# Kernel optimization log

Measured on AMD Instinct MI355X. Metric: run time of the kernel, lower is better.

## Reference

```python
import jax, jax.numpy as jnp
import numpy as np

EMBED_DIM = 512
KERNEL = 17


def setup_inputs() -> dict:
    key = jax.random.key(0)
    ks = jax.random.split(key, 5)
    B, L, C = 2, 8192, EMBED_DIM
    s = C ** -0.5
    x = jax.random.normal(ks[0], (B, L, C), dtype=jnp.float32)
    # weights stored as (in, out); equivalent to torch Linear weight.T
    w_qkv = jax.random.normal(ks[1], (C, 3 * C), dtype=jnp.float32) * s
    w_width = jax.random.normal(ks[2], (C, 1), dtype=jnp.float32) * s
    b_width = jax.random.normal(ks[3], (1,), dtype=jnp.float32) * 0.01
    w_out = jax.random.normal(ks[4], (C, C), dtype=jnp.float32) * s
    return {"x": x, "w_qkv": w_qkv, "w_width": w_width, "b_width": b_width, "w_out": w_out}


def reference(x, w_qkv, w_width, b_width, w_out):
    B, L, C = x.shape
    K = KERNEL
    half_k = K // 2
    scale = C ** -0.5

    qkv = x @ w_qkv                      # [B,L,3C]
    q, k, v = jnp.split(qkv, 3, axis=-1)

    # learned soft window width in [1, K]
    width = jax.nn.sigmoid(x @ w_width + b_width) * (K - 1) + 1.0   # [B,L,1]

    # sliding windows of k/v: pad along L then gather K-sized windows
    k_pad = jnp.pad(k, ((0, 0), (half_k, half_k), (0, 0)))
    v_pad = jnp.pad(v, ((0, 0), (half_k, half_k), (0, 0)))
    idx = jnp.arange(L)[:, None] + jnp.arange(K)[None, :]           # [L,K]
    k_win = k_pad[:, idx]                # [B,L,K,C]
    v_win = v_pad[:, idx]                # [B,L,K,C]

    scores = jnp.einsum('blc,blkc->blk', q, k_win) * scale          # [B,L,K]

    rel_pos = jnp.abs(jnp.arange(K, dtype=jnp.float32) - half_k)    # [K]
    soft_mask = jax.nn.sigmoid((width - rel_pos) * 5.0)             # [B,L,K]
    scores = scores - (1.0 - soft_mask) * 10000.0

    attn = jax.nn.softmax(scores, axis=-1)
    out = jnp.einsum('blk,blkc->blc', attn, v_win)                  # [B,L,C]
    return (out + v) @ w_out
```

## Files before the change

kernel.cpp:

```cpp
#include <hip/hip_runtime.h>

typedef unsigned short u16;
typedef unsigned int   u32;
typedef __attribute__((ext_vector_type(8))) short          shortx8;
typedef __attribute__((ext_vector_type(8))) unsigned short ushortx8;
typedef __attribute__((ext_vector_type(4))) float          floatx4;

#define AS1 __attribute__((address_space(1)))
#define AS3 __attribute__((address_space(3)))

#define SEG 8208
#define LV  16416

__device__ __forceinline__ float b2f(u16 v) {
  return __uint_as_float(((u32)v) << 16);
}
__device__ __forceinline__ u16 f2b(float f) {
  u32 u = __float_as_uint(f);
  u += 0x7FFF + ((u >> 16) & 1);
  return (u16)(u >> 16);
}
__device__ __forceinline__ void cp16(const void* g, void* l) {
  __builtin_amdgcn_global_load_lds((AS1 u32*)g, (AS3 u32*)l, 16, 0, 0);
}

__global__ __launch_bounds__(256)
void prep(const float* __restrict__ x, const float* __restrict__ w_width,
          const float* __restrict__ b_width, const float* __restrict__ w_qkv,
          const float* __restrict__ w_out, u16* __restrict__ xb,
          float* __restrict__ width, u16* __restrict__ wqkvT,
          u16* __restrict__ woutT, u16* __restrict__ Vt) {
  __shared__ u16 tile[32][33];
  const int b = blockIdx.x;
  if (b < 4096) {
    const int lane = threadIdx.x & 63;
    const int row  = b * 4 + (threadIdx.x >> 6);
    const float* xp = x + (size_t)row * 512 + lane * 8;
    floatx4 v0 = *(const floatx4*)xp;
    floatx4 v1 = *(const floatx4*)(xp + 4);
    floatx4 w0 = *(const floatx4*)(w_width + lane * 8);
    floatx4 w1 = *(const floatx4*)(w_width + lane * 8 + 4);
    float s = 0.f;
    ushortx8 o;
#pragma unroll
    for (int j = 0; j < 4; ++j) {
      s += v0[j] * w0[j] + v1[j] * w1[j];
      o[j] = f2b(v0[j]); o[4 + j] = f2b(v1[j]);
    }
    *(ushortx8*)(xb + (size_t)row * 512 + lane * 8) = o;
#pragma unroll
    for (int m = 32; m >= 1; m >>= 1) s += __shfl_xor(s, m, 64);
    if (lane == 0)
      width[row] = 16.f / (1.f + __expf(-(s + b_width[0]))) + 1.f;
  } else if (b < 5120) {
    const float* in; u16* out; int R, C, t;
    if (b < 4864) { in = w_qkv; out = wqkvT; R = 512; C = 1536; t = b - 4096; }
    else          { in = w_out; out = woutT; R = 512; C = 512;  t = b - 4864; }
    const int nbx = C / 32;
    const int cb = (t % nbx) * 32;
    const int rb = (t / nbx) * 32;
    const int tx = threadIdx.x & 31;
    const int ty = threadIdx.x >> 5;
#pragma unroll
    for (int i = 0; i < 32; i += 8)
      tile[ty + i][tx] = f2b(in[(size_t)(rb + ty + i) * C + cb + tx]);
    __syncthreads();
#pragma unroll
    for (int i = 0; i < 32; i += 8)
      out[(size_t)(cb + ty + i) * R + rb + tx] = tile[tx][ty + i];
  } else {
    const int idx = (b - 5120) * 256 + threadIdx.x;
    const int ch = idx >> 5;
    const int k  = idx & 31;
    const int seg = k >> 4;
    const int j   = k & 15;
    const int col = seg * SEG + (j < 8 ? j : 8192 + j);
    Vt[(size_t)ch * LV + col] = 0;
  }
}

template <int MODE>
__global__ __launch_bounds__(256, 3)
void gemm_bt(const u16* __restrict__ A, const u16* __restrict__ Bt,
             void* __restrict__ C0, u16* __restrict__ Kb, u16* __restrict__ Vt) {
  const int K = 512;
  __shared__ alignas(16) u16 lds[17408];
  u16* As = lds;
  u16* Bs = lds + 8192;
  const int tid  = threadIdx.x;
  const int lane = tid & 63;
  const int wave = tid >> 6;
  const int quad = lane >> 4;
  const int lr   = lane & 15;
  const int row0 = blockIdx.x * 128;
  const int col0 = blockIdx.y * 128;
  const int wr   = (wave >> 1) * 64;
  const int wc   = (wave & 1) * 64;

  floatx4 acc[4][4];
#pragma unroll
  for (int i = 0; i < 4; ++i)
#pragma unroll
    for (int j = 0; j < 4; ++j) acc[i][j] = (floatx4)0.0f;

  int srow[4], scol[4];
#pragma unroll
  for (int p = 0; p < 4; ++p) {
    int c = p * 256 + tid;
    srow[p] = c >> 3;
    scol[p] = ((c & 7) ^ (srow[p] & 7)) * 8;
  }
  const int swz = lr & 7;

  for (int k0 = 0; k0 < K; k0 += 64) {
#pragma unroll
    for (int p = 0; p < 4; ++p)
      cp16(A + (size_t)(row0 + srow[p]) * K + k0 + scol[p], &As[(p * 256 + tid) * 8]);
#pragma unroll
    for (int p = 0; p < 4; ++p)
      cp16(Bt + (size_t)(col0 + srow[p]) * K + k0 + scol[p], &Bs[(p * 256 + tid) * 8]);
    __syncthreads();

#pragma unroll
    for (int ks = 0; ks < 2; ++ks) {
      shortx8 af[4], bf[4];
#pragma unroll
      for (int mi = 0; mi < 4; ++mi)
        af[mi] = *(const shortx8*)
            &As[((wr + mi * 16 + lr) * 8 + ((ks * 4 + quad) ^ swz)) * 8];
#pragma unroll
      for (int ni = 0; ni < 4; ++ni)
        bf[ni] = *(const shortx8*)
            &Bs[((wc + ni * 16 + lr) * 8 + ((ks * 4 + quad) ^ swz)) * 8];
#pragma unroll
      for (int mi = 0; mi < 4; ++mi)
#pragma unroll
        for (int ni = 0; ni < 4; ++ni)
          acc[mi][ni] = __builtin_amdgcn_mfma_f32_16x16x32_bf16(
              af[mi], bf[ni], acc[mi][ni], 0, 0, 0);
    }
    __syncthreads();
  }

  if constexpr (MODE == 1) {
    if (col0 < 1024) {
      u16* dst = (col0 < 512) ? (u16*)C0 : Kb;
      const int cb = col0 & 511;
#pragma unroll
      for (int mi = 0; mi < 4; ++mi)
#pragma unroll
        for (int ni = 0; ni < 4; ++ni)
#pragma unroll
          for (int r = 0; r < 4; ++r)
            lds[(wr + mi * 16 + quad * 4 + r) * 136 + wc + ni * 16 + lr] =
                f2b(acc[mi][ni][r]);
      __syncthreads();
      const int rr = tid >> 4, cc = (tid & 15) * 8;
#pragma unroll
      for (int it = 0; it < 8; ++it) {
        int row = it * 16 + rr;
        *(ushortx8*)(dst + (size_t)(row0 + row) * 512 + cb + cc) =
            *(const ushortx8*)&lds[row * 136 + cc];
      }
    } else {
      const int cb = col0 - 1024;
      const int bb = row0 >> 13, pib0 = row0 & 8191;
#pragma unroll
      for (int mi = 0; mi < 4; ++mi)
#pragma unroll
        for (int ni = 0; ni < 4; ++ni)
#pragma unroll
          for (int r = 0; r < 4; ++r)
            lds[(wc + ni * 16 + lr) * 136 + wr + mi * 16 + quad * 4 + r] =
                f2b(acc[mi][ni][r]);
      __syncthreads();
      const int rr = tid >> 4, cc = (tid & 15) * 8;
#pragma unroll
      for (int it = 0; it < 8; ++it) {
        int chl = it * 16 + rr;
        ushortx8 v = *(const ushortx8*)&lds[chl * 136 + cc];
        *(ushortx8*)(Vt + (size_t)(cb + chl) * LV + (size_t)bb * SEG + 8 + pib0 + cc) = v;
      }
    }
  } else {
    float* Cf = (float*)C0;
#pragma unroll
    for (int mi = 0; mi < 4; ++mi)
#pragma unroll
      for (int ni = 0; ni < 4; ++ni)
#pragma unroll
        for (int r = 0; r < 4; ++r) {
          int row = row0 + wr + mi * 16 + quad * 4 + r;
          int col = col0 + wc + ni * 16 + lr;
          Cf[(size_t)row * 512 + col] = acc[mi][ni][r];
        }
  }
}

__global__ __launch_bounds__(256, 2)
void attn_fused(const u16* __restrict__ Q, const u16* __restrict__ Kb,
                const u16* __restrict__ Vt, const float* __restrict__ width,
                const u16* __restrict__ woutT, float* __restrict__ Out) {
  __shared__ alignas(16) u16 Osw[32 * 512];
  __shared__ float S[32][33];
  __shared__ u16 P[32][40];
  const int tid  = threadIdx.x;
  const int lane = tid & 63;
  const int wave = tid >> 6;
  const int quad = lane >> 4;
  const int lr   = lane & 15;
  const int p0   = blockIdx.x * 32;
  const int rg   = wave & 1;
  const int tw   = wave >> 1;
  const int prg  = p0 + rg * 16;
  const int pib  = prg & 8191;
  const int bb   = prg >> 13;

  floatx4 s0 = (floatx4)0.0f;
#pragma unroll 4
  for (int s = 0; s < 16; ++s) {
    const int k0 = s * 32 + quad * 8;
    shortx8 af = *(const shortx8*)(Q  + (size_t)(prg + lr) * 512 + k0);
    shortx8 f  = *(const shortx8*)(Kb +
                   (ptrdiff_t)(prg - 8 + tw * 16 + lr) * 512 + k0);
    s0 = __builtin_amdgcn_mfma_f32_16x16x32_bf16(af, f, s0, 0, 0, 0);
  }
#pragma unroll
  for (int r = 0; r < 4; ++r)
    S[rg * 16 + quad * 4 + r][tw * 16 + lr] = s0[r];
  __syncthreads();

  {
    const int row = tid >> 3, cg = tid & 7;
    const int rr  = row & 15;
    const int pibr = (p0 + (row >> 4) * 16) & 8191;
    const float scale = 0.044194173824159216f;
    const float wrow = width[p0 + row];
    float sv[4]; float mx = -1e30f;
#pragma unroll
    for (int t = 0; t < 4; ++t) {
      const int col = t * 8 + cg;
      const int d  = col - rr;
      const int jb = pibr + col - 8;
      float rel = fabsf((float)(d - 8));
      float msk = 1.f / (1.f + __expf(-5.f * (wrow - rel)));
      float pen = (1.f - msk) * 10000.f;
      float val = (d >= 0 && d <= 16)
          ? (((unsigned)jb < 8192u ? S[row][col] * scale : 0.f) - pen)
          : -1e30f;
      sv[t] = val; mx = fmaxf(mx, val);
    }
#pragma unroll
    for (int m = 4; m >= 1; m >>= 1) mx = fmaxf(mx, __shfl_xor(mx, m, 64));
    float e[4], sum = 0.f;
#pragma unroll
    for (int t = 0; t < 4; ++t) { e[t] = __expf(sv[t] - mx); sum += e[t]; }
#pragma unroll
    for (int m = 4; m >= 1; m >>= 1) sum += __shfl_xor(sum, m, 64);
    const float inv = 1.f / sum;
#pragma unroll
    for (int t = 0; t < 4; ++t) {
      const int col = t * 8 + cg;
      P[row][col] = f2b(e[t] * inv + ((col - rr) == 8 ? 1.f : 0.f));
    }
  }
  __syncthreads();

  shortx8 pf = *(const shortx8*)&P[rg * 16 + lr][quad * 8];
  const size_t cb0 = (size_t)bb * SEG + pib;
#pragma unroll 4
  for (int ctl = 0; ctl < 16; ++ctl) {
    const int ch = tw * 256 + ctl * 16 + lr;
    shortx8 vf = *(const shortx8*)(Vt + (size_t)ch * LV + cb0 + quad * 8);
    floatx4 o = __builtin_amdgcn_mfma_f32_16x16x32_bf16(pf, vf, (floatx4)0.0f,
                                                        0, 0, 0);
    const int c = tw * 32 + ctl * 2 + (lr >> 3);
#pragma unroll
    for (int r = 0; r < 4; ++r) {
      const int row = rg * 16 + quad * 4 + r;
      Osw[row * 512 + (((c & ~7) | ((c & 7) ^ (row & 7))) << 3) + (lr & 7)] =
          f2b(o[r]);
    }
  }
  __syncthreads();

  const int wc = wave * 128;
  floatx4 acc[2][8];
#pragma unroll
  for (int mi = 0; mi < 2; ++mi)
#pragma unroll
    for (int ni = 0; ni < 8; ++ni) acc[mi][ni] = (floatx4)0.0f;

  for (int ksl = 0; ksl < 16; ++ksl) {
    const int kg = ksl * 32 + quad * 8;
    shortx8 bfr[8], afr[2];
#pragma unroll
    for (int ni = 0; ni < 8; ++ni)
      bfr[ni] = *(const shortx8*)(woutT + (size_t)(wc + ni * 16 + lr) * 512 + kg);
#pragma unroll
    for (int mi = 0; mi < 2; ++mi) {
      const int row = mi * 16 + lr;
      const int c = ksl * 4 + quad;
      afr[mi] = *(const shortx8*)
          &Osw[row * 512 + (((c & ~7) | ((c & 7) ^ (row & 7))) << 3)];
    }
#pragma unroll
    for (int mi = 0; mi < 2; ++mi)
#pragma unroll
      for (int ni = 0; ni < 8; ++ni)
        acc[mi][ni] = __builtin_amdgcn_mfma_f32_16x16x32_bf16(
            afr[mi], bfr[ni], acc[mi][ni], 0, 0, 0);
  }

#pragma unroll
  for (int mi = 0; mi < 2; ++mi)
#pragma unroll
    for (int ni = 0; ni < 8; ++ni)
#pragma unroll
      for (int r = 0; r < 4; ++r)
        Out[(size_t)(p0 + mi * 16 + quad * 4 + r) * 512 + wc + ni * 16 + lr] =
            acc[mi][ni][r];
}

extern "C" void kernel_launch(void* const* d_in, const int* in_sizes, int n_in,
                              void* d_out, int out_size, void* d_ws, size_t ws_size,
                              hipStream_t stream) {
  const float* x       = (const float*)d_in[0];
  const float* w_qkv   = (const float*)d_in[1];
  const float* w_width = (const float*)d_in[2];
  const float* b_width = (const float*)d_in[3];
  const float* w_out   = (const float*)d_in[4];
  float* out = (float*)d_out;

  const int M = 16384, N3 = 1536;
  char* ws = (char*)d_ws;
  u16*   xb    = (u16*)(ws);
  u16*   Qb    = (u16*)(ws + 16777216);
  u16*   Kb    = (u16*)(ws + 33554432 + 8192);
  u16*   Vt    = (u16*)(ws + 50348032);
  u16*   wqkvT = (u16*)(ws + 67158016);
  u16*   woutT = (u16*)(ws + 68730880);
  float* width = (float*)(ws + 69255168);

  dim3 blk(256);
  prep<<<dim3(5184), blk, 0, stream>>>(x, w_width, b_width, w_qkv, w_out,
                                       xb, width, wqkvT, woutT, Vt);
  gemm_bt<1><<<dim3(M / 128, N3 / 128), blk, 0, stream>>>(xb, wqkvT, Qb, Kb, Vt);
  attn_fused<<<dim3(M / 32), blk, 0, stream>>>(Qb, Kb, Vt, width, woutT, out);
}
```

Measured before the change: 164.9 us.

## Double attn_fused block to 512 threads with split-K scores and register prefetch

The fused attention kernel now runs 8 waves per block instead of 4. The QK^T score computation is split across two K halves, with partial sums kept in shared memory and added during the softmax. The PV and output-projection work is spread over twice as many waves, each doing half as much. The output GEMM also prefetches the next K-slice of w_out fragments into registers to hide load latency. This aims to raise per-block parallelism and latency hiding, at the cost of extra shared memory for the partial scores and lower register budget per thread under the 512,4 launch bounds.

```diff
diff --git a/kernel.cpp b/kernel.cpp
--- a/kernel.cpp
+++ b/kernel.cpp
@@ -197,12 +197,12 @@
   }
 }
 
-__global__ __launch_bounds__(256, 2)
+__global__ __launch_bounds__(512, 4)
 void attn_fused(const u16* __restrict__ Q, const u16* __restrict__ Kb,
                 const u16* __restrict__ Vt, const float* __restrict__ width,
                 const u16* __restrict__ woutT, float* __restrict__ Out) {
   __shared__ alignas(16) u16 Osw[32 * 512];
-  __shared__ float S[32][33];
+  __shared__ float Sp[2][32][33];
   __shared__ u16 P[32][40];
   const int tid  = threadIdx.x;
   const int lane = tid & 63;
@@ -211,92 +211,104 @@
   const int lr   = lane & 15;
   const int p0   = blockIdx.x * 32;
   const int rg   = wave & 1;
-  const int tw   = wave >> 1;
+  const int tw   = (wave >> 1) & 1;
+  const int kh   = wave >> 2;
+  const int cw   = wave >> 1;
   const int prg  = p0 + rg * 16;
   const int pib  = prg & 8191;
   const int bb   = prg >> 13;
 
-  floatx4 s0 = (floatx4)0.0f;
-#pragma unroll 4
-  for (int s = 0; s < 16; ++s) {
-    const int k0 = s * 32 + quad * 8;
-    shortx8 af = *(const shortx8*)(Q  + (size_t)(prg + lr) * 512 + k0);
-    shortx8 f  = *(const shortx8*)(Kb +
-                   (ptrdiff_t)(prg - 8 + tw * 16 + lr) * 512 + k0);
-    s0 = __builtin_amdgcn_mfma_f32_16x16x32_bf16(af, f, s0, 0, 0, 0);
-  }
-#pragma unroll
-  for (int r = 0; r < 4; ++r)
-    S[rg * 16 + quad * 4 + r][tw * 16 + lr] = s0[r];
+  {
+    const u16* qb = Q  + (size_t)(prg + lr) * 512 + kh * 256 + quad * 8;
+    const u16* kb = Kb + (ptrdiff_t)(prg - 8 + tw * 16 + lr) * 512 +
+                    kh * 256 + quad * 8;
+    floatx4 s0 = (floatx4)0.0f;
+#pragma unroll
+    for (int s = 0; s < 8; ++s) {
+      shortx8 af = *(const shortx8*)(qb + s * 32);
+      shortx8 f  = *(const shortx8*)(kb + s * 32);
+      s0 = __builtin_amdgcn_mfma_f32_16x16x32_bf16(af, f, s0, 0, 0, 0);
+    }
+#pragma unroll
+    for (int r = 0; r < 4; ++r)
+      Sp[kh][rg * 16 + quad * 4 + r][tw * 16 + lr] = s0[r];
+  }
   __syncthreads();
 
   {
-    const int row = tid >> 3, cg = tid & 7;
+    const int row = tid >> 4, cg = tid & 15;
     const int rr  = row & 15;
     const int pibr = (p0 + (row >> 4) * 16) & 8191;
     const float scale = 0.044194173824159216f;
     const float wrow = width[p0 + row];
-    float sv[4]; float mx = -1e30f;
-#pragma unroll
-    for (int t = 0; t < 4; ++t) {
-      const int col = t * 8 + cg;
+    float sv[2]; float mx = -1e30f;
+#pragma unroll
+    for (int t = 0; t < 2; ++t) {
+      const int col = t * 16 + cg;
       const int d  = col - rr;
       const int jb = pibr + col - 8;
+      float s = Sp[0][row][col] + Sp[1][row][col];
       float rel = fabsf((float)(d - 8));
       float msk = 1.f / (1.f + __expf(-5.f * (wrow - rel)));
       float pen = (1.f - msk) * 10000.f;
       float val = (d >= 0 && d <= 16)
-          ? (((unsigned)jb < 8192u ? S[row][col] * scale : 0.f) - pen)
+          ? (((unsigned)jb < 8192u ? s * scale : 0.f) - pen)
           : -1e30f;
       sv[t] = val; mx = fmaxf(mx, val);
     }
 #pragma unroll
-    for (int m = 4; m >= 1; m >>= 1) mx = fmaxf(mx, __shfl_xor(mx, m, 64));
-    float e[4], sum = 0.f;
-#pragma unroll
-    for (int t = 0; t < 4; ++t) { e[t] = __expf(sv[t] - mx); sum += e[t]; }
-#pragma unroll
-    for (int m = 4; m >= 1; m >>= 1) sum += __shfl_xor(sum, m, 64);
+    for (int m = 8; m >= 1; m >>= 1) mx = fmaxf(mx, __shfl_xor(mx, m, 64));
+    float e0 = __expf(sv[0] - mx), e1 = __expf(sv[1] - mx);
+    float sum = e0 + e1;
+#pragma unroll
+    for (int m = 8; m >= 1; m >>= 1) sum += __shfl_xor(sum, m, 64);
     const float inv = 1.f / sum;
-#pragma unroll
-    for (int t = 0; t < 4; ++t) {
-      const int col = t * 8 + cg;
-      P[row][col] = f2b(e[t] * inv + ((col - rr) == 8 ? 1.f : 0.f));
-    }
+    P[row][cg]      = f2b(e0 * inv + ((cg - rr) == 8 ? 1.f : 0.f));
+    P[row][cg + 16] = f2b(e1 * inv + ((cg + 16 - rr) == 8 ? 1.f : 0.f));
   }
   __syncthreads();
 
-  shortx8 pf = *(const shortx8*)&P[rg * 16 + lr][quad * 8];
-  const size_t cb0 = (size_t)bb * SEG + pib;
-#pragma unroll 4
-  for (int ctl = 0; ctl < 16; ++ctl) {
-    const int ch = tw * 256 + ctl * 16 + lr;
-    shortx8 vf = *(const shortx8*)(Vt + (size_t)ch * LV + cb0 + quad * 8);
-    floatx4 o = __builtin_amdgcn_mfma_f32_16x16x32_bf16(pf, vf, (floatx4)0.0f,
-                                                        0, 0, 0);
-    const int c = tw * 32 + ctl * 2 + (lr >> 3);
-#pragma unroll
-    for (int r = 0; r < 4; ++r) {
-      const int row = rg * 16 + quad * 4 + r;
-      Osw[row * 512 + (((c & ~7) | ((c & 7) ^ (row & 7))) << 3) + (lr & 7)] =
-          f2b(o[r]);
+  {
+    shortx8 pf = *(const shortx8*)&P[rg * 16 + lr][quad * 8];
+    const size_t cb0 = (size_t)bb * SEG + pib;
+#pragma unroll
+    for (int ct = 0; ct < 8; ++ct) {
+      const int ch = cw * 128 + ct * 16 + lr;
+      shortx8 vf = *(const shortx8*)(Vt + (size_t)ch * LV + cb0 + quad * 8);
+      floatx4 o = __builtin_amdgcn_mfma_f32_16x16x32_bf16(pf, vf, (floatx4)0.0f,
+                                                          0, 0, 0);
+      const int c = cw * 16 + ct * 2 + (lr >> 3);
+#pragma unroll
+      for (int r = 0; r < 4; ++r) {
+        const int row = rg * 16 + quad * 4 + r;
+        Osw[row * 512 + (((c & ~7) | ((c & 7) ^ (row & 7))) << 3) + (lr & 7)] =
+            f2b(o[r]);
+      }
     }
   }
   __syncthreads();
 
-  const int wc = wave * 128;
-  floatx4 acc[2][8];
+  const int wc = wave * 64;
+  const u16* wbase = woutT + (size_t)(wc + lr) * 512 + quad * 8;
+  floatx4 acc[2][4];
 #pragma unroll
   for (int mi = 0; mi < 2; ++mi)
 #pragma unroll
-    for (int ni = 0; ni < 8; ++ni) acc[mi][ni] = (floatx4)0.0f;
+    for (int ni = 0; ni < 4; ++ni) acc[mi][ni] = (floatx4)0.0f;
+
+  shortx8 bcur[4], bnxt[4];
+#pragma unroll
+  for (int ni = 0; ni < 4; ++ni)
+    bcur[ni] = *(const shortx8*)(wbase + (size_t)ni * 16 * 512);
 
   for (int ksl = 0; ksl < 16; ++ksl) {
-    const int kg = ksl * 32 + quad * 8;
-    shortx8 bfr[8], afr[2];
-#pragma unroll
-    for (int ni = 0; ni < 8; ++ni)
-      bfr[ni] = *(const shortx8*)(woutT + (size_t)(wc + ni * 16 + lr) * 512 + kg);
+    if (ksl < 15) {
+#pragma unroll
+      for (int ni = 0; ni < 4; ++ni)
+        bnxt[ni] = *(const shortx8*)(wbase + (size_t)ni * 16 * 512 +
+                                     (ksl + 1) * 32);
+    }
+    shortx8 afr[2];
 #pragma unroll
     for (int mi = 0; mi < 2; ++mi) {
       const int row = mi * 16 + lr;
@@ -307,15 +319,17 @@
 #pragma unroll
     for (int mi = 0; mi < 2; ++mi)
 #pragma unroll
-      for (int ni = 0; ni < 8; ++ni)
+      for (int ni = 0; ni < 4; ++ni)
         acc[mi][ni] = __builtin_amdgcn_mfma_f32_16x16x32_bf16(
-            afr[mi], bfr[ni], acc[mi][ni], 0, 0, 0);
+            afr[mi], bcur[ni], acc[mi][ni], 0, 0, 0);
+#pragma unroll
+    for (int ni = 0; ni < 4; ++ni) bcur[ni] = bnxt[ni];
   }
 
 #pragma unroll
   for (int mi = 0; mi < 2; ++mi)
 #pragma unroll
-    for (int ni = 0; ni < 8; ++ni)
+    for (int ni = 0; ni < 4; ++ni)
 #pragma unroll
       for (int r = 0; r < 4; ++r)
         Out[(size_t)(p0 + mi * 16 + quad * 4 + r) * 512 + wc + ni * 16 + lr] =
@@ -342,9 +356,10 @@
   u16*   woutT = (u16*)(ws + 68730880);
   float* width = (float*)(ws + 69255168);
 
-  dim3 blk(256);
-  prep<<<dim3(5184), blk, 0, stream>>>(x, w_width, b_width, w_qkv, w_out,
-                                       xb, width, wqkvT, woutT, Vt);
-  gemm_bt<1><<<dim3(M / 128, N3 / 128), blk, 0, stream>>>(xb, wqkvT, Qb, Kb, Vt);
-  attn_fused<<<dim3(M / 32), blk, 0, stream>>>(Qb, Kb, Vt, width, woutT, out);
-}
+  prep<<<dim3(5184), dim3(256), 0, stream>>>(x, w_width, b_width, w_qkv, w_out,
+                                             xb, width, wqkvT, woutT, Vt);
+  gemm_bt<1><<<dim3(M / 128, N3 / 128), dim3(256), 0, stream>>>(xb, wqkvT, Qb,
+                                                                Kb, Vt);
+  attn_fused<<<dim3(M / 32), dim3(512), 0, stream>>>(Qb, Kb, Vt, width, woutT,
+                                                     out);
+}
```

New measurement: 164.5 us. No clear change (-0.2%).
